# Kernel optimization log

Hardware: AMD Instinct MI355X
Metric: run time of the kernel (lower is better)

Reference implementation:

```python
import jax, jax.numpy as jnp
import numpy as np

N = 50000       # nodes
E = 800000      # edges (before self-loops)
B = 1024        # graphs
D = 256         # emb = hidden = representation size
OUT = 128
NFEAT = 9       # OGB atom features
VOCAB = 100
NLAYERS = 4     # 1 + hidden_layers(2) + 1
NEG_SLOPE = 0.2


def setup_inputs() -> dict:
    key = jax.random.key(0)
    ks = jax.random.split(key, 10)
    x = jax.random.randint(ks[0], (N, NFEAT), 0, VOCAB)
    edge_index = jax.random.randint(ks[1], (2, E), 0, N)
    batch = jnp.sort(jax.random.randint(ks[2], (N,), 0, B))
    atom_emb = jax.random.normal(ks[3], (NFEAT, VOCAB, D), jnp.float32) * 0.1
    Ws = jax.random.normal(ks[4], (NLAYERS, D, D), jnp.float32) * (1.0 / np.sqrt(D))
    a_src = jax.random.normal(ks[5], (NLAYERS, D), jnp.float32) * 0.1
    a_dst = jax.random.normal(ks[6], (NLAYERS, D), jnp.float32) * 0.1
    biases = jnp.zeros((NLAYERS, D), jnp.float32)
    lin_w = jax.random.normal(ks[7], (3 * D, OUT), jnp.float32) * (1.0 / np.sqrt(3 * D))
    lin_b = jnp.zeros((OUT,), jnp.float32)
    return dict(x=x, edge_index=edge_index, batch=batch, atom_emb=atom_emb,
                Ws=Ws, a_src=a_src, a_dst=a_dst, biases=biases,
                lin_w=lin_w, lin_b=lin_b)


def _gat_layer(h, src, dst, W, asrc, adst, b):
    # PyG GATConv, heads=1: linear transform, per-edge additive attention,
    # segment softmax over incoming edges of each target, scatter-add aggregate.
    h = h @ W                                        # [N, D]
    s = jnp.einsum('nd,d->n', h, asrc)               # source-side score
    t = jnp.einsum('nd,d->n', h, adst)               # target-side score
    e = jax.nn.leaky_relu(s[src] + t[dst], NEG_SLOPE)  # [E']
    m = jax.ops.segment_max(e, dst, num_segments=N)  # segment softmax (stable)
    e = jnp.exp(e - m[dst])
    denom = jax.ops.segment_sum(e, dst, num_segments=N)
    alpha = e / denom[dst]                           # self-loops ensure denom > 0
    out = jax.ops.segment_sum(alpha[:, None] * h[src], dst, num_segments=N)
    return out + b


def reference(x, edge_index, batch, atom_emb, Ws, a_src, a_dst, biases, lin_w, lin_b):
    # AtomEncoder: sum of per-feature embedding lookups -> [N, D]
    h = atom_emb[jnp.arange(NFEAT)[:, None], x.T].sum(axis=0)
    # add self-loops once (GATConv default add_self_loops=True)
    loops = jnp.arange(N)
    src = jnp.concatenate([edge_index[0], loops])
    dst = jnp.concatenate([edge_index[1], loops])
    for l in range(NLAYERS):
        h = _gat_layer(h, src, dst, Ws[l], a_src[l], a_dst[l], biases[l])
        h = jax.nn.relu(h)
    # global mean / add / max pooling over graphs
    count = jax.ops.segment_sum(jnp.ones((N,), h.dtype), batch, num_segments=B)
    x_add = jax.ops.segment_sum(h, batch, num_segments=B)
    x_mean = x_add / jnp.maximum(count, 1.0)[:, None]
    x_max = jax.ops.segment_max(h, batch, num_segments=B)
    x_max = jnp.where(count[:, None] > 0, x_max, 0.0)
    feats = jnp.concatenate([x_mean, x_add, x_max], axis=1)  # [B, 3D]
    # dropout is identity in eval mode
    return feats @ lin_w + lin_b
```

## Files before the change

### kernel.cpp

```cpp
#include <hip/hip_runtime.h>
#include <math.h>

#define N_NODES 50000
#define N_EDGES 800000
#define NGRAPH  1024
#define D       256
#define OUTD    128
#define NFEAT   9
#define VOCABSZ 100
#define NLAYERS 4
#define NEG_SLOPE 0.2f
#define MAXD    64
#define SEED_NBLK ((N_NODES + 255) / 256)
#define WT_NBLK (NLAYERS * D * D / 256)
#define ATOM_NBLK ((N_NODES + 3) / 4)
#define SCAT_NBLK ((N_EDGES + 255) / 256)
#define GROW_NBLK ((N_NODES + 255) / 256)

typedef __attribute__((ext_vector_type(8))) short short8;
typedef __attribute__((ext_vector_type(4))) float f32x4;
typedef __attribute__((ext_vector_type(2))) float f32x2;

static __device__ __forceinline__ unsigned short f2bf(float f) {
    unsigned int u = __float_as_uint(f);
    u = (u + 0x7FFFu + ((u >> 16) & 1u)) >> 16;
    return (unsigned short)u;
}
static __device__ __forceinline__ float bf2f(unsigned short u) {
    return __uint_as_float(((unsigned int)u) << 16);
}

#define GLOAD_LDS16(g, l) __builtin_amdgcn_global_load_lds( \
    (const __attribute__((address_space(1))) void*)(g), \
    (__attribute__((address_space(3))) void*)(l), 16, 0, 0)

__global__ void seed_kernel(int* __restrict__ cnt, int* __restrict__ ell) {
    int i = blockIdx.x * blockDim.x + threadIdx.x;
    if (i < N_NODES) {
        cnt[i] = 1;
        ell[i << 6] = i;
    }
}

__global__ __launch_bounds__(256) void init_scatter_fused(int* __restrict__ cnt,
                                                          int* __restrict__ ell,
                                                          const float* __restrict__ W,
                                                          unsigned short* __restrict__ Wt,
                                                          const int* __restrict__ x,
                                                          const float* __restrict__ emb,
                                                          unsigned short* __restrict__ h,
                                                          const int* __restrict__ src,
                                                          const int* __restrict__ dst,
                                                          const int* __restrict__ batch,
                                                          int* __restrict__ growptr) {
    int b = blockIdx.x;
    if (b < SCAT_NBLK) {
        int e = b * 256 + threadIdx.x;
        if (e < N_EDGES) {
            int d = dst[e];
            int pos = atomicAdd(&cnt[d], 1);
            if (pos < MAXD) ell[(d << 6) + pos] = src[e];
        }
    } else if (b < SCAT_NBLK + ATOM_NBLK) {
        int node = (b - SCAT_NBLK) * 4 + (threadIdx.x >> 6);
        int lane = threadIdx.x & 63;
        if (node >= N_NODES) return;
        float4 acc = make_float4(0.f, 0.f, 0.f, 0.f);
        #pragma unroll
        for (int f = 0; f < NFEAT; ++f) {
            int xi = x[node * NFEAT + f];
            float4 v = *(const float4*)&emb[(size_t)(f * VOCABSZ + xi) * D + lane * 4];
            acc.x += v.x; acc.y += v.y; acc.z += v.z; acc.w += v.w;
        }
        ushort4 o;
        o.x = f2bf(acc.x); o.y = f2bf(acc.y); o.z = f2bf(acc.z); o.w = f2bf(acc.w);
        *(ushort4*)&h[node * D + lane * 4] = o;
    } else if (b < SCAT_NBLK + ATOM_NBLK + WT_NBLK) {
        int t = (b - SCAT_NBLK - ATOM_NBLK) * 256 + threadIdx.x;
        int l = t >> 16;
        int k = (t >> 8) & 255;
        int n = t & 255;
        Wt[(l << 16) + n * 256 + k] = f2bf(W[t]);
    } else {
        int n = (b - SCAT_NBLK - ATOM_NBLK - WT_NBLK) * 256 + threadIdx.x;
        if (n >= N_NODES) return;
        int bb = batch[n];
        int prev = (n == 0) ? -1 : batch[n - 1];
        for (int g = prev + 1; g <= bb; ++g) growptr[g] = n;
        if (n == N_NODES - 1) {
            for (int g = bb + 1; g <= NGRAPH; ++g) growptr[g] = N_NODES;
        }
    }
}

#define GBM 128
#define GBK 64
__global__ __launch_bounds__(512) void gemm_bf16(const unsigned short* __restrict__ A,
                                                 const unsigned short* __restrict__ Wt,
                                                 const float* __restrict__ asrc,
                                                 const float* __restrict__ adst,
                                                 unsigned short* __restrict__ C,
                                                 float* __restrict__ s_out,
                                                 float* __restrict__ t_out) {
    __shared__ unsigned short smem[33792];
    __shared__ float s_sh[GBM], t_sh[GBM];
    int row0 = blockIdx.x * GBM;
    int tid = threadIdx.x;
    int wid = tid >> 6;
    int lane = tid & 63;
    int wm = wid >> 2, wn = wid & 3;
    int l15 = lane & 15;
    int lhi = lane >> 4;

    if (tid < GBM) s_sh[tid] = 0.f;
    else if (tid < 2 * GBM) t_sh[tid - GBM] = 0.f;

    int srcA[2], srcB[4];
    #pragma unroll
    for (int q = 0; q < 2; ++q) {
        int slot = q * 512 + tid;
        int r = slot >> 3, c = slot & 7;
        int ra = row0 + r; if (ra > N_NODES - 1) ra = N_NODES - 1;
        srcA[q] = ra * D + ((c ^ (r & 7)) << 3);
    }
    #pragma unroll
    for (int q = 0; q < 4; ++q) {
        int slot = q * 512 + tid;
        int r = slot >> 3, c = slot & 7;
        srcB[q] = r * D + ((c ^ (r & 7)) << 3);
    }

    f32x4 acc[4][4];
    #pragma unroll
    for (int i = 0; i < 4; ++i)
        #pragma unroll
        for (int j = 0; j < 4; ++j) acc[i][j] = (f32x4){0.f, 0.f, 0.f, 0.f};

    #pragma unroll
    for (int step = 0; step < 4; ++step) {
        int k0 = step * GBK;
        #pragma unroll
        for (int q = 0; q < 2; ++q)
            GLOAD_LDS16(A + srcA[q] + k0, &smem[(q * 512 + wid * 64) * 8]);
        #pragma unroll
        for (int q = 0; q < 4; ++q)
            GLOAD_LDS16(Wt + srcB[q] + k0, &smem[8192 + (q * 512 + wid * 64) * 8]);
        __syncthreads();
        #pragma unroll
        for (int ks = 0; ks < 2; ++ks) {
            short8 af[4], bf[4];
            #pragma unroll
            for (int m = 0; m < 4; ++m) {
                int r = wm * 64 + m * 16 + l15;
                int c = ks * 4 + lhi;
                af[m] = *(const short8*)&smem[r * GBK + ((c ^ (r & 7)) << 3)];
            }
            #pragma unroll
            for (int n = 0; n < 4; ++n) {
                int r = wn * 64 + n * 16 + l15;
                int c = ks * 4 + lhi;
                bf[n] = *(const short8*)&smem[8192 + r * GBK + ((c ^ (r & 7)) << 3)];
            }
            #pragma unroll
            for (int m = 0; m < 4; ++m)
                #pragma unroll
                for (int n = 0; n < 4; ++n)
                    acc[m][n] = __builtin_amdgcn_mfma_f32_16x16x32_bf16(af[m], bf[n], acc[m][n], 0, 0, 0);
        }
        __syncthreads();
    }

    unsigned short* c_s = smem;
    #pragma unroll
    for (int m = 0; m < 4; ++m) {
        #pragma unroll
        for (int r = 0; r < 4; ++r) {
            int lr = wm * 64 + m * 16 + lhi * 4 + r;
            #pragma unroll
            for (int n = 0; n < 4; ++n) {
                int lc = wn * 64 + n * 16 + l15;
                c_s[lr * 264 + lc] = f2bf(acc[m][n][r]);
            }
        }
    }
    __syncthreads();
    #pragma unroll
    for (int p = 0; p < 8; ++p) {
        int slot = p * 512 + tid;
        int r2 = slot >> 5;
        int c2 = slot & 31;
        int grow = row0 + r2;
        if (grow < N_NODES) {
            short8 vv = *(const short8*)&c_s[r2 * 264 + c2 * 8];
            *(short8*)&C[(size_t)grow * D + c2 * 8] = vv;
        }
    }

    float av[4], bv[4];
    #pragma unroll
    for (int n = 0; n < 4; ++n) {
        int gcol = wn * 64 + n * 16 + l15;
        av[n] = asrc[gcol];
        bv[n] = adst[gcol];
    }
    #pragma unroll
    for (int m = 0; m < 4; ++m) {
        #pragma unroll
        for (int r = 0; r < 4; ++r) {
            float ps = 0.f, pt = 0.f;
            #pragma unroll
            for (int n = 0; n < 4; ++n) {
                ps += acc[m][n][r] * av[n];
                pt += acc[m][n][r] * bv[n];
            }
            #pragma unroll
            for (int off = 1; off < 16; off <<= 1) {
                ps += __shfl_xor(ps, off, 64);
                pt += __shfl_xor(pt, off, 64);
            }
            if (l15 == 0) {
                int lr = wm * 64 + m * 16 + lhi * 4 + r;
                atomicAdd(&s_sh[lr], ps);
                atomicAdd(&t_sh[lr], pt);
            }
        }
    }
    __syncthreads();
    if (tid < GBM) {
        int gr = row0 + tid;
        if (gr < N_NODES) s_out[gr] = s_sh[tid];
    } else if (tid < 2 * GBM) {
        int gr = row0 + tid - GBM;
        if (gr < N_NODES) t_out[gr] = t_sh[tid - GBM];
    }
}

__global__ __launch_bounds__(256) void aggregate_kernel(const unsigned short* __restrict__ hW,
                                                        const float* __restrict__ s,
                                                        const float* __restrict__ t,
                                                        const int* __restrict__ cnt,
                                                        const int* __restrict__ ell,
                                                        const float* __restrict__ bias,
                                                        unsigned short* __restrict__ hout) {
    int v = (blockIdx.x * blockDim.x + threadIdx.x) >> 6;
    int lane = threadIdx.x & 63;
    if (v >= N_NODES) return;
    int beg = v << 6;
    int deg = cnt[v]; if (deg > MAXD) deg = MAXD;
    float tv = t[v];
    float m = -1e30f;
    float denom = 0.f;
    f32x2 acc2[4];
    #pragma unroll
    for (int j = 0; j < 4; ++j) acc2[j] = (f32x2){0.f, 0.f};
    int half = lane >> 5;
    int l32 = lane & 31;
    const unsigned short* hbase = hW + (size_t)l32 * 8;

    for (int base = 0; base < deg; base += 64) {
        int rem = deg - base; if (rem > 64) rem = 64;
        int u = 0; float e = -1e30f;
        if (lane < rem) {
            u = ell[beg + base + lane];
            float ev = s[u] + tv;
            e = (ev > 0.f) ? ev : NEG_SLOPE * ev;
        }
        float cm = e;
        #pragma unroll
        for (int off = 32; off; off >>= 1) cm = fmaxf(cm, __shfl_xor(cm, off, 64));
        float newm = fmaxf(m, cm);
        float scale = __expf(m - newm);
        float p = (lane < rem) ? __expf(e - newm) : 0.f;
        float ws = p;
        #pragma unroll
        for (int off = 32; off; off >>= 1) ws += __shfl_xor(ws, off, 64);
        denom = denom * scale + ws;
        m = newm;
        f32x2 sc2 = (f32x2){scale, scale};
        #pragma unroll
        for (int j = 0; j < 4; ++j) acc2[j] *= sc2;
        for (int i = 0; i < rem; i += 4) {
            int idx0 = i + half;
            int idx1 = i + 2 + half;
            float p0 = __shfl(p, idx0, 64);
            int   u0 = __shfl(u, idx0, 64);
            float p1 = __shfl(p, idx1, 64);
            int   u1 = __shfl(u, idx1, 64);
            uint4 w0 = *(const uint4*)(hbase + ((size_t)u0 << 8));
            uint4 w1 = *(const uint4*)(hbase + ((size_t)u1 << 8));
            f32x2 p20 = (f32x2){p0, p0};
            f32x2 p21 = (f32x2){p1, p1};
            unsigned int ww; f32x2 h2;
            ww = w0.x; h2 = (f32x2){__uint_as_float(ww << 16), __uint_as_float(ww & 0xffff0000u)};
            acc2[0] += p20 * h2;
            ww = w0.y; h2 = (f32x2){__uint_as_float(ww << 16), __uint_as_float(ww & 0xffff0000u)};
            acc2[1] += p20 * h2;
            ww = w0.z; h2 = (f32x2){__uint_as_float(ww << 16), __uint_as_float(ww & 0xffff0000u)};
            acc2[2] += p20 * h2;
            ww = w0.w; h2 = (f32x2){__uint_as_float(ww << 16), __uint_as_float(ww & 0xffff0000u)};
            acc2[3] += p20 * h2;
            ww = w1.x; h2 = (f32x2){__uint_as_float(ww << 16), __uint_as_float(ww & 0xffff0000u)};
            acc2[0] += p21 * h2;
            ww = w1.y; h2 = (f32x2){__uint_as_float(ww << 16), __uint_as_float(ww & 0xffff0000u)};
            acc2[1] += p21 * h2;
            ww = w1.z; h2 = (f32x2){__uint_as_float(ww << 16), __uint_as_float(ww & 0xffff0000u)};
            acc2[2] += p21 * h2;
            ww = w1.w; h2 = (f32x2){__uint_as_float(ww << 16), __uint_as_float(ww & 0xffff0000u)};
            acc2[3] += p21 * h2;
        }
    }
    #pragma unroll
    for (int j = 0; j < 4; ++j) {
        acc2[j].x += __shfl_xor(acc2[j].x, 32, 64);
        acc2[j].y += __shfl_xor(acc2[j].y, 32, 64);
    }
    float inv = 1.f / denom;
    if (half == 0) {
        float4 b0 = *(const float4*)&bias[l32 * 8];
        float4 b1 = *(const float4*)&bias[l32 * 8 + 4];
        float bb[8] = {b0.x, b0.y, b0.z, b0.w, b1.x, b1.y, b1.z, b1.w};
        float av[8] = {acc2[0].x, acc2[0].y, acc2[1].x, acc2[1].y,
                       acc2[2].x, acc2[2].y, acc2[3].x, acc2[3].y};
        short8 o;
        #pragma unroll
        for (int j = 0; j < 8; ++j) {
            float val = fmaxf(av[j] * inv + bb[j], 0.f);
            o[j] = (short)f2bf(val);
        }
        *(short8*)&hout[(size_t)v * D + l32 * 8] = o;
    }
}

__global__ __launch_bounds__(256) void pool_kernel(const unsigned short* __restrict__ h,
                                                   const int* __restrict__ growptr,
                                                   float* __restrict__ feats) {
    int g = blockIdx.x;
    int wid = threadIdx.x >> 6;
    int lane = threadIdx.x & 63;
    int beg = growptr[g], end = growptr[g + 1];
    float4 add = make_float4(0.f, 0.f, 0.f, 0.f);
    float4 mx = make_float4(-1e30f, -1e30f, -1e30f, -1e30f);
    for (int v = beg + wid; v < end; v += 4) {
        ushort4 hv = *(const ushort4*)&h[(size_t)v * D + lane * 4];
        float a0 = bf2f(hv.x), a1 = bf2f(hv.y), a2 = bf2f(hv.z), a3 = bf2f(hv.w);
        add.x += a0; add.y += a1; add.z += a2; add.w += a3;
        mx.x = fmaxf(mx.x, a0); mx.y = fmaxf(mx.y, a1);
        mx.z = fmaxf(mx.z, a2); mx.w = fmaxf(mx.w, a3);
    }
    __shared__ float sadd[4][D];
    __shared__ float smax[4][D];
    *(float4*)&sadd[wid][lane * 4] = add;
    *(float4*)&smax[wid][lane * 4] = mx;
    __syncthreads();
    if (wid == 0) {
        float4 A0 = *(const float4*)&sadd[0][lane * 4];
        float4 A1 = *(const float4*)&sadd[1][lane * 4];
        float4 A2 = *(const float4*)&sadd[2][lane * 4];
        float4 A3 = *(const float4*)&sadd[3][lane * 4];
        float4 M0 = *(const float4*)&smax[0][lane * 4];
        float4 M1 = *(const float4*)&smax[1][lane * 4];
        float4 M2 = *(const float4*)&smax[2][lane * 4];
        float4 M3 = *(const float4*)&smax[3][lane * 4];
        float4 ta = make_float4(A0.x + A1.x + A2.x + A3.x, A0.y + A1.y + A2.y + A3.y,
                                A0.z + A1.z + A2.z + A3.z, A0.w + A1.w + A2.w + A3.w);
        float4 tm = make_float4(fmaxf(fmaxf(M0.x, M1.x), fmaxf(M2.x, M3.x)),
                                fmaxf(fmaxf(M0.y, M1.y), fmaxf(M2.y, M3.y)),
                                fmaxf(fmaxf(M0.z, M1.z), fmaxf(M2.z, M3.z)),
                                fmaxf(fmaxf(M0.w, M1.w), fmaxf(M2.w, M3.w)));
        float cnt = (float)(end - beg);
        float invc = 1.f / fmaxf(cnt, 1.f);
        if (cnt <= 0.f) tm = make_float4(0.f, 0.f, 0.f, 0.f);
        float4 mean = make_float4(ta.x * invc, ta.y * invc, ta.z * invc, ta.w * invc);
        float* fr = feats + (size_t)g * 3 * D;
        *(float4*)&fr[0 * D + 4 * lane] = mean;
        *(float4*)&fr[1 * D + 4 * lane] = ta;
        *(float4*)&fr[2 * D + 4 * lane] = tm;
    }
}

__global__ __launch_bounds__(512) void final_linear(const float* __restrict__ feats,
                                                    const float* __restrict__ lw,
                                                    const float* __restrict__ lb,
                                                    float* __restrict__ out) {
    int g = blockIdx.x;
    int tid = threadIdx.x;
    int kq = tid >> 7;
    int j = tid & 127;
    __shared__ float sf[3 * D];
    __shared__ float sacc[4][OUTD];
    for (int i = tid; i < 3 * D; i += 512) sf[i] = feats[(size_t)g * 3 * D + i];
    __syncthreads();
    float acc = 0.f;
    const float* lwp = lw + (kq * 192) * OUTD + j;
    const float* sfp = sf + kq * 192;
    #pragma unroll 8
    for (int i = 0; i < 192; ++i)
        acc += sfp[i] * lwp[i * OUTD];
    sacc[kq][j] = acc;
    __syncthreads();
    if (kq == 0)
        out[g * OUTD + j] = lb[j] + sacc[0][j] + sacc[1][j] + sacc[2][j] + sacc[3][j];
}

extern "C" void kernel_launch(void* const* d_in, const int* in_sizes, int n_in,
                              void* d_out, int out_size, void* d_ws, size_t ws_size,
                              hipStream_t stream) {
    const int*   x        = (const int*)d_in[0];
    const int*   edge_idx = (const int*)d_in[1];
    const int*   batch    = (const int*)d_in[2];
    const float* atom_emb = (const float*)d_in[3];
    const float* Ws       = (const float*)d_in[4];
    const float* a_src    = (const float*)d_in[5];
    const float* a_dst    = (const float*)d_in[6];
    const float* biases   = (const float*)d_in[7];
    const float* lin_w    = (const float*)d_in[8];
    const float* lin_b    = (const float*)d_in[9];
    float* out = (float*)d_out;

    char* ws = (char*)d_ws;
    size_t off = 0;
    auto alloc = [&](size_t bytes) -> void* {
        void* p = ws + off;
        off += (bytes + 255) & ~(size_t)255;
        return p;
    };
    unsigned short* bufA  = (unsigned short*)alloc(sizeof(short) * (size_t)N_NODES * D);
    unsigned short* bufB  = (unsigned short*)alloc(sizeof(short) * (size_t)N_NODES * D);
    unsigned short* Wt    = (unsigned short*)alloc(sizeof(short) * NLAYERS * D * D);
    float* s      = (float*)alloc(sizeof(float) * N_NODES);
    float* t      = (float*)alloc(sizeof(float) * N_NODES);
    int*   cnt    = (int*)alloc(sizeof(int) * N_NODES);
    int*   ell    = (int*)alloc(sizeof(int) * (size_t)N_NODES * MAXD);
    int*   growp  = (int*)alloc(sizeof(int) * (NGRAPH + 1));
    float* feats  = (float*)alloc(sizeof(float) * (size_t)NGRAPH * 3 * D);

    const int* esrc = edge_idx;
    const int* edst = edge_idx + N_EDGES;

    seed_kernel<<<SEED_NBLK, 256, 0, stream>>>(cnt, ell);
    init_scatter_fused<<<SCAT_NBLK + ATOM_NBLK + WT_NBLK + GROW_NBLK, 256, 0, stream>>>(
        cnt, ell, Ws, Wt, x, atom_emb, bufA, esrc, edst, batch, growp);

    for (int l = 0; l < NLAYERS; ++l) {
        gemm_bf16<<<(N_NODES + GBM - 1) / GBM, 512, 0, stream>>>(
                                             bufA, Wt + (size_t)l * D * D,
                                             a_src + l * D, a_dst + l * D,
                                             bufB, s, t);
        aggregate_kernel<<<(N_NODES + 3) / 4, 256, 0, stream>>>(bufB, s, t,
                                             cnt, ell, biases + l * D, bufA);
    }

    pool_kernel<<<NGRAPH, 256, 0, stream>>>(bufA, growp, feats);
    final_linear<<<NGRAPH, 512, 0, stream>>>(feats, lin_w, lin_b, out);
}
```

Before: 439.6 us.

## Fold seed into init kernel and overlap edge scatter with first GEMM

The separate seed kernel is merged into the init kernel's graph-pointer branch, which drops one launch. The edge-scatter work (atomic ELL construction) moves out of the init kernel and into extra blocks of the layer-0 GEMM launch, so it can run alongside the GEMM tiles. This cuts the init kernel's block count and hides scatter latency behind GEMM compute. The trade-off is that scatter blocks now run at 512 threads and carry the GEMM kernel's LDS allocation, which may reduce how many of them fit on a CU at once.

Result: no change. 444.4 us (+1.1%).

```diff
diff --git a/kernel.cpp b/kernel.cpp
--- a/kernel.cpp
+++ b/kernel.cpp
@@ -11,11 +11,13 @@
 #define NLAYERS 4
 #define NEG_SLOPE 0.2f
 #define MAXD    64
-#define SEED_NBLK ((N_NODES + 255) / 256)
 #define WT_NBLK (NLAYERS * D * D / 256)
 #define ATOM_NBLK ((N_NODES + 3) / 4)
-#define SCAT_NBLK ((N_EDGES + 255) / 256)
-#define GROW_NBLK ((N_NODES + 255) / 256)
+#define SEEDGROW_NBLK ((N_NODES + 255) / 256)
+#define GBM 128
+#define GBK 64
+#define NGB ((N_NODES + GBM - 1) / GBM)
+#define SCAT512 ((N_EDGES + 511) / 512)
 
 typedef __attribute__((ext_vector_type(8))) short short8;
 typedef __attribute__((ext_vector_type(4))) float f32x4;
@@ -34,35 +36,18 @@
     (const __attribute__((address_space(1))) void*)(g), \
     (__attribute__((address_space(3))) void*)(l), 16, 0, 0)
 
-__global__ void seed_kernel(int* __restrict__ cnt, int* __restrict__ ell) {
-    int i = blockIdx.x * blockDim.x + threadIdx.x;
-    if (i < N_NODES) {
-        cnt[i] = 1;
-        ell[i << 6] = i;
-    }
-}
-
-__global__ __launch_bounds__(256) void init_scatter_fused(int* __restrict__ cnt,
-                                                          int* __restrict__ ell,
-                                                          const float* __restrict__ W,
-                                                          unsigned short* __restrict__ Wt,
-                                                          const int* __restrict__ x,
-                                                          const float* __restrict__ emb,
-                                                          unsigned short* __restrict__ h,
-                                                          const int* __restrict__ src,
-                                                          const int* __restrict__ dst,
-                                                          const int* __restrict__ batch,
-                                                          int* __restrict__ growptr) {
+__global__ __launch_bounds__(256) void init_fused(int* __restrict__ cnt,
+                                                  int* __restrict__ ell,
+                                                  const float* __restrict__ W,
+                                                  unsigned short* __restrict__ Wt,
+                                                  const int* __restrict__ x,
+                                                  const float* __restrict__ emb,
+                                                  unsigned short* __restrict__ h,
+                                                  const int* __restrict__ batch,
+                                                  int* __restrict__ growptr) {
     int b = blockIdx.x;
-    if (b < SCAT_NBLK) {
-        int e = b * 256 + threadIdx.x;
-        if (e < N_EDGES) {
-            int d = dst[e];
-            int pos = atomicAdd(&cnt[d], 1);
-            if (pos < MAXD) ell[(d << 6) + pos] = src[e];
-        }
-    } else if (b < SCAT_NBLK + ATOM_NBLK) {
-        int node = (b - SCAT_NBLK) * 4 + (threadIdx.x >> 6);
+    if (b < ATOM_NBLK) {
+        int node = b * 4 + (threadIdx.x >> 6);
         int lane = threadIdx.x & 63;
         if (node >= N_NODES) return;
         float4 acc = make_float4(0.f, 0.f, 0.f, 0.f);
@@ -75,15 +60,17 @@
         ushort4 o;
         o.x = f2bf(acc.x); o.y = f2bf(acc.y); o.z = f2bf(acc.z); o.w = f2bf(acc.w);
         *(ushort4*)&h[node * D + lane * 4] = o;
-    } else if (b < SCAT_NBLK + ATOM_NBLK + WT_NBLK) {
-        int t = (b - SCAT_NBLK - ATOM_NBLK) * 256 + threadIdx.x;
+    } else if (b < ATOM_NBLK + WT_NBLK) {
+        int t = (b - ATOM_NBLK) * 256 + threadIdx.x;
         int l = t >> 16;
         int k = (t >> 8) & 255;
         int n = t & 255;
         Wt[(l << 16) + n * 256 + k] = f2bf(W[t]);
     } else {
-        int n = (b - SCAT_NBLK - ATOM_NBLK - WT_NBLK) * 256 + threadIdx.x;
+        int n = (b - ATOM_NBLK - WT_NBLK) * 256 + threadIdx.x;
         if (n >= N_NODES) return;
+        cnt[n] = 1;
+        ell[n << 6] = n;
         int bb = batch[n];
         int prev = (n == 0) ? -1 : batch[n - 1];
         for (int g = prev + 1; g <= bb; ++g) growptr[g] = n;
@@ -93,9 +80,8 @@
     }
 }
 
-#define GBM 128
-#define GBK 64
-__global__ __launch_bounds__(512) void gemm_bf16(const unsigned short* __restrict__ A,
+static __device__ __forceinline__ void gemm_body(int bid,
+                                                 const unsigned short* __restrict__ A,
                                                  const unsigned short* __restrict__ Wt,
                                                  const float* __restrict__ asrc,
                                                  const float* __restrict__ adst,
@@ -104,7 +90,7 @@
                                                  float* __restrict__ t_out) {
     __shared__ unsigned short smem[33792];
     __shared__ float s_sh[GBM], t_sh[GBM];
-    int row0 = blockIdx.x * GBM;
+    int row0 = bid * GBM;
     int tid = threadIdx.x;
     int wid = tid >> 6;
     int lane = tid & 63;
@@ -232,6 +218,40 @@
     } else if (tid < 2 * GBM) {
         int gr = row0 + tid - GBM;
         if (gr < N_NODES) t_out[gr] = t_sh[tid - GBM];
+    }
+}
+
+__global__ __launch_bounds__(512) void gemm_bf16(const unsigned short* __restrict__ A,
+                                                 const unsigned short* __restrict__ Wt,
+                                                 const float* __restrict__ asrc,
+                                                 const float* __restrict__ adst,
+                                                 unsigned short* __restrict__ C,
+                                                 float* __restrict__ s_out,
+                                                 float* __restrict__ t_out) {
+    gemm_body(blockIdx.x, A, Wt, asrc, adst, C, s_out, t_out);
+}
+
+__global__ __launch_bounds__(512) void gemm0_scatter(const unsigned short* __restrict__ A,
+                                                     const unsigned short* __restrict__ Wt,
+                                                     const float* __restrict__ asrc,
+                                                     const float* __restrict__ adst,
+                                                     unsigned short* __restrict__ C,
+                                                     float* __restrict__ s_out,
+                                                     float* __restrict__ t_out,
+                                                     const int* __restrict__ src,
+                                                     const int* __restrict__ dst,
+                                                     int* __restrict__ cnt,
+                                                     int* __restrict__ ell) {
+    int b = blockIdx.x;
+    if (b < NGB) {
+        gemm_body(b, A, Wt, asrc, adst, C, s_out, t_out);
+    } else {
+        int e = (b - NGB) * 512 + threadIdx.x;
+        if (e < N_EDGES) {
+            int d = dst[e];
+            int pos = atomicAdd(&cnt[d], 1);
+            if (pos < MAXD) ell[(d << 6) + pos] = src[e];
+        }
     }
 }
 
@@ -437,15 +457,18 @@
     const int* esrc = edge_idx;
     const int* edst = edge_idx + N_EDGES;
 
-    seed_kernel<<<SEED_NBLK, 256, 0, stream>>>(cnt, ell);
-    init_scatter_fused<<<SCAT_NBLK + ATOM_NBLK + WT_NBLK + GROW_NBLK, 256, 0, stream>>>(
-        cnt, ell, Ws, Wt, x, atom_emb, bufA, esrc, edst, batch, growp);
+    init_fused<<<ATOM_NBLK + WT_NBLK + SEEDGROW_NBLK, 256, 0, stream>>>(
+        cnt, ell, Ws, Wt, x, atom_emb, bufA, batch, growp);
 
     for (int l = 0; l < NLAYERS; ++l) {
-        gemm_bf16<<<(N_NODES + GBM - 1) / GBM, 512, 0, stream>>>(
-                                             bufA, Wt + (size_t)l * D * D,
-                                             a_src + l * D, a_dst + l * D,
-                                             bufB, s, t);
+        if (l == 0) {
+            gemm0_scatter<<<NGB + SCAT512, 512, 0, stream>>>(
+                bufA, Wt, a_src, a_dst, bufB, s, t, esrc, edst, cnt, ell);
+        } else {
+            gemm_bf16<<<NGB, 512, 0, stream>>>(
+                bufA, Wt + (size_t)l * D * D,
+                a_src + l * D, a_dst + l * D, bufB, s, t);
+        }
         aggregate_kernel<<<(N_NODES + 3) / 4, 256, 0, stream>>>(bufB, s, t,
                                              cnt, ell, biases + l * D, bufA);
     }
```
